# Performance work log

Hardware: AMD Instinct MI355X
Metric: run time of the kernel (lower is better)

The kernel has to match this reference:

```python
import jax, jax.numpy as jnp
import numpy as np

EPS = 1e-8

def setup_inputs() -> dict:
    key = jax.random.key(0)
    k1, k2 = jax.random.split(key)
    B, T = 512, 65536
    preds = jax.random.normal(k1, (B, T), dtype=jnp.float32)
    labels = jax.random.normal(k2, (B, T), dtype=jnp.float32)
    return {"preds": preds, "labels": labels}

def reference(preds, labels):
    # Batched per-sample statistics over all non-batch dims (here last axis).
    mean_x = jnp.mean(preds, axis=1)                      # [B]
    mean_y = jnp.mean(labels, axis=1)                     # [B]
    xc = preds - mean_x[:, None]
    yc = labels - mean_y[:, None]
    var_x = jnp.mean(xc * xc, axis=1)
    var_y = jnp.mean(yc * yc, axis=1)
    cov_xy = jnp.mean(xc * yc, axis=1)
    ccc = 2.0 * cov_xy / (var_x + var_y + (mean_x - mean_y) ** 2 + EPS)
    return jnp.mean(1.0 - ccc)
```

## Files before the change

### kernel.cpp

```cpp
#include <hip/hip_runtime.h>

#define CCC_EPS 1e-8

__global__ __launch_bounds__(1024) void ccc_row_kernel(
    const float* __restrict__ preds,
    const float* __restrict__ labels,
    float* __restrict__ row_loss,
    int T)
{
    const int b = blockIdx.x;
    const size_t base = (size_t)b * (size_t)T;
    const float4* __restrict__ p4 = (const float4*)(preds + base);
    const float4* __restrict__ l4 = (const float4*)(labels + base);
    const int n4 = T >> 2;

    float sx = 0.f, sy = 0.f, sxx = 0.f, syy = 0.f, sxy = 0.f;

    #pragma unroll 4
    for (int i = threadIdx.x; i < n4; i += 1024) {
        float4 x = p4[i];
        float4 y = l4[i];
        sx  += x.x + x.y + x.z + x.w;
        sy  += y.x + y.y + y.z + y.w;
        sxx = fmaf(x.x, x.x, sxx); sxx = fmaf(x.y, x.y, sxx);
        sxx = fmaf(x.z, x.z, sxx); sxx = fmaf(x.w, x.w, sxx);
        syy = fmaf(y.x, y.x, syy); syy = fmaf(y.y, y.y, syy);
        syy = fmaf(y.z, y.z, syy); syy = fmaf(y.w, y.w, syy);
        sxy = fmaf(x.x, y.x, sxy); sxy = fmaf(x.y, y.y, sxy);
        sxy = fmaf(x.z, y.z, sxy); sxy = fmaf(x.w, y.w, sxy);
    }

    #pragma unroll
    for (int off = 32; off > 0; off >>= 1) {
        sx  += __shfl_down(sx,  off);
        sy  += __shfl_down(sy,  off);
        sxx += __shfl_down(sxx, off);
        syy += __shfl_down(syy, off);
        sxy += __shfl_down(sxy, off);
    }

    __shared__ float red[16][5];
    const int wave = threadIdx.x >> 6;
    const int lane = threadIdx.x & 63;
    if (lane == 0) {
        red[wave][0] = sx;  red[wave][1] = sy;  red[wave][2] = sxx;
        red[wave][3] = syy; red[wave][4] = sxy;
    }
    __syncthreads();

    if (threadIdx.x == 0) {
        double tsx = 0, tsy = 0, tsxx = 0, tsyy = 0, tsxy = 0;
        #pragma unroll
        for (int w = 0; w < 16; ++w) {
            tsx  += red[w][0];
            tsy  += red[w][1];
            tsxx += red[w][2];
            tsyy += red[w][3];
            tsxy += red[w][4];
        }
        const double inv = 1.0 / (double)T;
        const double mx = tsx * inv;
        const double my = tsy * inv;
        const double vx = tsxx * inv - mx * mx;
        const double vy = tsyy * inv - my * my;
        const double cov = tsxy * inv - mx * my;
        const double d = mx - my;
        const double ccc = 2.0 * cov / (vx + vy + d * d + CCC_EPS);
        row_loss[b] = (float)(1.0 - ccc);
    }
}

__global__ __launch_bounds__(512) void ccc_final_kernel(
    const float* __restrict__ row_loss,
    float* __restrict__ out,
    int B)
{
    float s = 0.f;
    for (int i = threadIdx.x; i < B; i += 512) s += row_loss[i];
    #pragma unroll
    for (int off = 32; off > 0; off >>= 1) s += __shfl_down(s, off);

    __shared__ float red[8];
    const int wave = threadIdx.x >> 6;
    const int lane = threadIdx.x & 63;
    if (lane == 0) red[wave] = s;
    __syncthreads();
    if (threadIdx.x == 0) {
        float t = 0.f;
        #pragma unroll
        for (int w = 0; w < 8; ++w) t += red[w];
        out[0] = t / (float)B;
    }
}

extern "C" void kernel_launch(void* const* d_in, const int* in_sizes, int n_in,
                              void* d_out, int out_size, void* d_ws, size_t ws_size,
                              hipStream_t stream) {
    const float* preds  = (const float*)d_in[0];
    const float* labels = (const float*)d_in[1];
    float* out = (float*)d_out;

    const int T = 65536;
    const int B = in_sizes[0] / T;

    float* row_loss = (float*)d_ws;

    ccc_row_kernel<<<B, 1024, 0, stream>>>(preds, labels, row_loss, T);
    ccc_final_kernel<<<1, 512, 0, stream>>>(row_loss, out, B);
}
```

Measured before the change: 277.6 us.

## Split each row across multiple blocks with fully unrolled upfront loads

Each row is divided into 8 segments, each handled by a 256-thread block that issues all its float4 loads before accumulating. The blocks write per-segment partial sums, and the final kernel combines segments per row in double precision and then averages the losses. This raises the block count and the number of memory requests in flight to better saturate HBM bandwidth. It assumes T is exactly 8*256*8*4, so other sizes would break.

Result: faster. 271.4 us (-2.2%).

```diff
diff --git a/kernel.cpp b/kernel.cpp
--- a/kernel.cpp
+++ b/kernel.cpp
@@ -1,25 +1,34 @@
 #include <hip/hip_runtime.h>
 
 #define CCC_EPS 1e-8
+#define SEGS 8
+#define K_UNROLL 8
 
-__global__ __launch_bounds__(1024) void ccc_row_kernel(
+__global__ __launch_bounds__(256) void ccc_partial_kernel(
     const float* __restrict__ preds,
     const float* __restrict__ labels,
-    float* __restrict__ row_loss,
+    float* __restrict__ partial,
     int T)
 {
-    const int b = blockIdx.x;
-    const size_t base = (size_t)b * (size_t)T;
-    const float4* __restrict__ p4 = (const float4*)(preds + base);
-    const float4* __restrict__ l4 = (const float4*)(labels + base);
-    const int n4 = T >> 2;
+    const int seg = blockIdx.x;
+    const int row = blockIdx.y;
+    const int seg4 = (T >> 2) / SEGS;
+    const size_t base4 = (size_t)row * (size_t)(T >> 2) + (size_t)seg * seg4;
+    const float4* __restrict__ p4 = (const float4*)preds + base4;
+    const float4* __restrict__ l4 = (const float4*)labels + base4;
+
+    float4 xs[K_UNROLL], ys[K_UNROLL];
+    #pragma unroll
+    for (int k = 0; k < K_UNROLL; ++k) {
+        xs[k] = p4[threadIdx.x + k * 256];
+        ys[k] = l4[threadIdx.x + k * 256];
+    }
 
     float sx = 0.f, sy = 0.f, sxx = 0.f, syy = 0.f, sxy = 0.f;
-
-    #pragma unroll 4
-    for (int i = threadIdx.x; i < n4; i += 1024) {
-        float4 x = p4[i];
-        float4 y = l4[i];
+    #pragma unroll
+    for (int k = 0; k < K_UNROLL; ++k) {
+        float4 x = xs[k];
+        float4 y = ys[k];
         sx  += x.x + x.y + x.z + x.w;
         sy  += y.x + y.y + y.z + y.w;
         sxx = fmaf(x.x, x.x, sxx); sxx = fmaf(x.y, x.y, sxx);
@@ -39,7 +48,7 @@
         sxy += __shfl_down(sxy, off);
     }
 
-    __shared__ float red[16][5];
+    __shared__ float red[4][5];
     const int wave = threadIdx.x >> 6;
     const int lane = threadIdx.x & 63;
     if (lane == 0) {
@@ -49,14 +58,32 @@
     __syncthreads();
 
     if (threadIdx.x == 0) {
+        float t0 = red[0][0] + red[1][0] + red[2][0] + red[3][0];
+        float t1 = red[0][1] + red[1][1] + red[2][1] + red[3][1];
+        float t2 = red[0][2] + red[1][2] + red[2][2] + red[3][2];
+        float t3 = red[0][3] + red[1][3] + red[2][3] + red[3][3];
+        float t4 = red[0][4] + red[1][4] + red[2][4] + red[3][4];
+        float* dst = partial + ((size_t)row * SEGS + seg) * 5;
+        dst[0] = t0; dst[1] = t1; dst[2] = t2; dst[3] = t3; dst[4] = t4;
+    }
+}
+
+__global__ __launch_bounds__(512) void ccc_final_kernel(
+    const float* __restrict__ partial,
+    float* __restrict__ out,
+    int B, int T)
+{
+    float loss_sum = 0.f;
+    for (int b = threadIdx.x; b < B; b += 512) {
         double tsx = 0, tsy = 0, tsxx = 0, tsyy = 0, tsxy = 0;
+        const float* src = partial + (size_t)b * SEGS * 5;
         #pragma unroll
-        for (int w = 0; w < 16; ++w) {
-            tsx  += red[w][0];
-            tsy  += red[w][1];
-            tsxx += red[w][2];
-            tsyy += red[w][3];
-            tsxy += red[w][4];
+        for (int s = 0; s < SEGS; ++s) {
+            tsx  += src[s * 5 + 0];
+            tsy  += src[s * 5 + 1];
+            tsxx += src[s * 5 + 2];
+            tsyy += src[s * 5 + 3];
+            tsxy += src[s * 5 + 4];
         }
         const double inv = 1.0 / (double)T;
         const double mx = tsx * inv;
@@ -66,24 +93,16 @@
         const double cov = tsxy * inv - mx * my;
         const double d = mx - my;
         const double ccc = 2.0 * cov / (vx + vy + d * d + CCC_EPS);
-        row_loss[b] = (float)(1.0 - ccc);
+        loss_sum += (float)(1.0 - ccc);
     }
-}
 
-__global__ __launch_bounds__(512) void ccc_final_kernel(
-    const float* __restrict__ row_loss,
-    float* __restrict__ out,
-    int B)
-{
-    float s = 0.f;
-    for (int i = threadIdx.x; i < B; i += 512) s += row_loss[i];
     #pragma unroll
-    for (int off = 32; off > 0; off >>= 1) s += __shfl_down(s, off);
+    for (int off = 32; off > 0; off >>= 1) loss_sum += __shfl_down(loss_sum, off);
 
     __shared__ float red[8];
     const int wave = threadIdx.x >> 6;
     const int lane = threadIdx.x & 63;
-    if (lane == 0) red[wave] = s;
+    if (lane == 0) red[wave] = loss_sum;
     __syncthreads();
     if (threadIdx.x == 0) {
         float t = 0.f;
@@ -103,8 +122,9 @@
     const int T = 65536;
     const int B = in_sizes[0] / T;
 
-    float* row_loss = (float*)d_ws;
+    float* partial = (float*)d_ws;
 
-    ccc_row_kernel<<<B, 1024, 0, stream>>>(preds, labels, row_loss, T);
-    ccc_final_kernel<<<1, 512, 0, stream>>>(row_loss, out, B);
+    dim3 grid(SEGS, B);
+    ccc_partial_kernel<<<grid, 256, 0, stream>>>(preds, labels, partial, T);
+    ccc_final_kernel<<<1, 512, 0, stream>>>(partial, out, B, T);
 }
```
